# Optimization experiments

Measured on AMD Instinct MI355X. Metric: run time of the kernel, lower is better.

## Reference

```python
import jax, jax.numpy as jnp
import numpy as np

N_NODES = 50000
N_EDGES = 800000
IN_C, HID_C, OUT_C = 256, 256, 128


def gcn_conv(x, W, b, row, col, n_nodes):
    """PyG GCNConv: linear transform, symmetric-normalized aggregation, bias.
    row/col already include self-loops. Messages flow row -> col."""
    h = x @ W  # [N, out]
    deg = jax.ops.segment_sum(jnp.ones_like(col, dtype=h.dtype), col, num_segments=n_nodes)
    d_inv_sqrt = jnp.where(deg > 0, jax.lax.rsqrt(jnp.maximum(deg, 1e-12)), 0.0)
    norm = d_inv_sqrt[row] * d_inv_sqrt[col]  # [E]
    msg = h[row] * norm[:, None]              # gather + scale, [E, out]
    out = jax.ops.segment_sum(msg, col, num_segments=n_nodes)  # scatter-add
    return out + b


def setup_inputs() -> dict:
    key = jax.random.key(0)
    k_x, k_e, k_w1, k_w2 = jax.random.split(key, 4)
    x = jax.random.normal(k_x, (N_NODES, IN_C), dtype=jnp.float32)
    edge_index = jax.random.randint(k_e, (2, N_EDGES), 0, N_NODES, dtype=jnp.int64)
    # Glorot-style init for GCN weights, zeros bias (PyG default)
    s1 = float(np.sqrt(6.0 / (IN_C + HID_C)))
    s2 = float(np.sqrt(6.0 / (HID_C + OUT_C)))
    W1 = jax.random.uniform(k_w1, (IN_C, HID_C), dtype=jnp.float32, minval=-s1, maxval=s1)
    b1 = jnp.zeros((HID_C,), dtype=jnp.float32)
    W2 = jax.random.uniform(k_w2, (HID_C, OUT_C), dtype=jnp.float32, minval=-s2, maxval=s2)
    b2 = jnp.zeros((OUT_C,), dtype=jnp.float32)
    return {"x": x, "edge_index": edge_index, "W1": W1, "b1": b1, "W2": W2, "b2": b2}


def reference(x, edge_index, W1, b1, W2, b2):
    n = x.shape[0]
    # add self-loops (PyG GCNConv default add_self_loops=True)
    loops = jnp.arange(n, dtype=edge_index.dtype)
    row = jnp.concatenate([edge_index[0], loops])
    col = jnp.concatenate([edge_index[1], loops])
    h = gcn_conv(x, W1, b1, row, col, n)
    h = jax.nn.relu(h)  # dropout p=0.0 -> identity
    out = gcn_conv(h, W2, b2, row, col, n)
    return out
```

## Files before the change

### kernel.cpp

```cpp
#include <hip/hip_runtime.h>

#define NN 50000
#define NE 800000
#define IN_C 256
#define HID_C 256
#define OUT_C 128

#define NETP (NE + 8 * NN)
#define NBUCK 196
#define CHUNK 4096
#define NPA 196
#define CAP_B 6400

typedef unsigned short u16;
typedef unsigned int u32;
typedef __attribute__((ext_vector_type(8))) short short8;
typedef __attribute__((ext_vector_type(8))) unsigned short ushort8;
typedef __attribute__((ext_vector_type(4))) float f32x4;
typedef __attribute__((ext_vector_type(2))) float f32x2;
typedef __attribute__((ext_vector_type(4))) unsigned u32x4;

#define CPS ((size_t)(NN + 1) * 32)

__device__ __forceinline__ u16 f2b(float f) {
  unsigned int u = __float_as_uint(f);
  return (u16)((u + 0x7FFFu + ((u >> 16) & 1u)) >> 16);
}
__device__ __forceinline__ float b2f(u16 s) {
  return __uint_as_float(((unsigned int)s) << 16);
}


__global__ __launch_bounds__(256) void convw_zero(const float* __restrict__ W1,
                                                  const float* __restrict__ W2,
                                                  u16* __restrict__ W1t,
                                                  u16* __restrict__ W2t,
                                                  int* __restrict__ cnt,
                                                  u16* __restrict__ Hb,
                                                  int nzb) {
  int b = blockIdx.x;
  if (b < 256) {
    int id = b * 256 + threadIdx.x;
    if (id < 256 * 256) {
      int n = id >> 8, k = id & 255;
      W1t[id] = f2b(W1[k * 256 + n]);
    }
    if (id < 128 * 256) {
      int n = id >> 8, k = id & 255;
      W2t[id] = f2b(W2[k * 128 + n]);
    }
  } else if (b < 256 + nzb) {
    int i = (b - 256) * 256 + threadIdx.x;
    if (i < NN) cnt[i] = 1;
  } else {
    int t = threadIdx.x;
    Hb[(size_t)(t >> 5) * CPS + (size_t)NN * 32 + (t & 31)] = 0;
  }
}


__global__ __launch_bounds__(256) void hist_kernel(const int* __restrict__ col,
                                                   int* __restrict__ cnt, int E) {
  int e = blockIdx.x * blockDim.x + threadIdx.x;
  if (e < E) atomicAdd(&cnt[col[e]], 1);
}

__global__ __launch_bounds__(256) void scan1_kernel(const int* __restrict__ cnt,
                                                    int* __restrict__ bsum, int n) {
  __shared__ int ws[4];
  int i = blockIdx.x * 256 + threadIdx.x;
  int lane = threadIdx.x & 63, wid = threadIdx.x >> 6;
  int v = (i < n) ? ((cnt[i] + 7) & ~7) : 0;
#pragma unroll
  for (int off = 32; off > 0; off >>= 1) v += __shfl_down(v, off, 64);
  if (lane == 0) ws[wid] = v;
  __syncthreads();
  if (threadIdx.x == 0) bsum[blockIdx.x] = ws[0] + ws[1] + ws[2] + ws[3];
}

__global__ __launch_bounds__(256) void scan2_kernel(const int* __restrict__ bsum,
                                                    int* __restrict__ boff,
                                                    int* __restrict__ row_off,
                                                    int nb, int n) {
  __shared__ int wsum[4], wpre[5];
  int lane = threadIdx.x & 63, wid = threadIdx.x >> 6;
  int v = (threadIdx.x < nb) ? bsum[threadIdx.x] : 0;
  int s = v;
#pragma unroll
  for (int off = 1; off < 64; off <<= 1) {
    int t = __shfl_up(s, off, 64);
    if (lane >= off) s += t;
  }
  if (lane == 63) wsum[wid] = s;
  __syncthreads();
  if (threadIdx.x == 0) {
    int acc = 0;
#pragma unroll
    for (int w = 0; w < 4; ++w) { wpre[w] = acc; acc += wsum[w]; }
    wpre[4] = acc;
  }
  __syncthreads();
  if (threadIdx.x < nb) boff[threadIdx.x] = wpre[wid] + (s - v);
  if (threadIdx.x == 0) row_off[n] = wpre[4];
}

__global__ __launch_bounds__(256) void scan3_kernel(const int* __restrict__ cnt,
                                                    const int* __restrict__ boff,
                                                    int* __restrict__ row_off,
                                                    int* __restrict__ bcur,
                                                    float* __restrict__ dinv, int n) {
  __shared__ int wsum[4], wpre[4];
  int i = blockIdx.x * 256 + threadIdx.x;
  int lane = threadIdx.x & 63, wid = threadIdx.x >> 6;
  int vr = (i < n) ? cnt[i] : 0;
  int v = (vr + 7) & ~7;
  int s = v;
#pragma unroll
  for (int off = 1; off < 64; off <<= 1) {
    int t = __shfl_up(s, off, 64);
    if (lane >= off) s += t;
  }
  if (lane == 63) wsum[wid] = s;
  __syncthreads();
  if (threadIdx.x == 0) {
    int acc = 0;
#pragma unroll
    for (int w = 0; w < 4; ++w) { wpre[w] = acc; acc += wsum[w]; }
  }
  __syncthreads();
  if (i < n) {
    int off = boff[blockIdx.x] + wpre[wid] + (s - v);
    row_off[i] = off;
    if ((i & 255) == 0) bcur[i >> 8] = off;
    dinv[i] = rsqrtf((float)vr);
  }
}


template <bool A_IS_F32, bool PLANAR_C>
__device__ __forceinline__ void gemm_body(const void* __restrict__ Ap,
                                          const u16* __restrict__ Bt,
                                          const float* __restrict__ dscale,
                                          u16* __restrict__ C, int M, int N,
                                          int bx, int by,
                                          u16 (&Asl)[2][5120], u16 (&Bsl)[2][5120]) {
  const int tid = threadIdx.x;
  const int row0 = by * 128;
  const int col0 = bx * 128;

  f32x4 acc[4][4] = {};

  const int seg = tid & 7;
  const int rb = tid >> 3;
  const int wave = tid >> 6, lane = tid & 63;
  const int wm = wave >> 1, wn = wave & 1;
  const int qr = lane & 15, quad = lane >> 4;

  float4 aF[4];
  ushort4 aU[4];
  ushort4 bR[4];

  auto load_tiles = [&](int k0) {
    if constexpr (A_IS_F32) {
      const float* A = (const float*)Ap;
#pragma unroll
      for (int i = 0; i < 4; ++i) {
        int gr = row0 + rb + i * 32;
        aF[i] = (gr < M) ? *(const float4*)&A[(size_t)gr * 256 + k0 + seg * 4]
                         : make_float4(0.f, 0.f, 0.f, 0.f);
      }
    } else {
      const u16* A = (const u16*)Ap;
#pragma unroll
      for (int i = 0; i < 4; ++i) {
        int gr = row0 + rb + i * 32;
        aU[i] = (gr < M) ? *(const ushort4*)&A[(size_t)gr * 256 + k0 + seg * 4]
                         : make_ushort4(0, 0, 0, 0);
      }
    }
#pragma unroll
    for (int i = 0; i < 4; ++i) {
      int n = rb + i * 32;
      bR[i] = *(const ushort4*)&Bt[(size_t)(col0 + n) * 256 + k0 + seg * 4];
    }
  };

  auto write_lds = [&](int buf) {
#pragma unroll
    for (int i = 0; i < 4; ++i) {
      int r = rb + i * 32;
      ushort4 u;
      if constexpr (A_IS_F32) {
        u.x = f2b(aF[i].x); u.y = f2b(aF[i].y);
        u.z = f2b(aF[i].z); u.w = f2b(aF[i].w);
      } else {
        u = aU[i];
      }
      *(ushort4*)&Asl[buf][r * 40 + seg * 4] = u;
      *(ushort4*)&Bsl[buf][r * 40 + seg * 4] = bR[i];
    }
  };

  load_tiles(0);
  write_lds(0);
  __syncthreads();

#pragma unroll
  for (int it = 0; it < 8; ++it) {
    const int cur = it & 1;
    if (it < 7) load_tiles((it + 1) * 32);

    short8 afr[4], bfr[4];
#pragma unroll
    for (int mt = 0; mt < 4; ++mt)
      afr[mt] = *(const short8*)&Asl[cur][(wm * 64 + mt * 16 + qr) * 40 + quad * 8];
#pragma unroll
    for (int nt = 0; nt < 4; ++nt)
      bfr[nt] = *(const short8*)&Bsl[cur][(wn * 64 + nt * 16 + qr) * 40 + quad * 8];
#pragma unroll
    for (int mt = 0; mt < 4; ++mt)
#pragma unroll
      for (int nt = 0; nt < 4; ++nt)
        acc[mt][nt] = __builtin_amdgcn_mfma_f32_16x16x32_bf16(afr[mt], bfr[nt], acc[mt][nt], 0, 0, 0);

    if (it < 7) {
      write_lds(1 - cur);
      __syncthreads();
    }
  }

#pragma unroll
  for (int mt = 0; mt < 4; ++mt) {
#pragma unroll
    for (int i = 0; i < 4; ++i) {
      int gr = row0 + wm * 64 + mt * 16 + quad * 4 + i;
      if (gr < M) {
        float sc = dscale[gr];
#pragma unroll
        for (int nt = 0; nt < 4; ++nt) {
          int gc = col0 + wn * 64 + nt * 16 + qr;
          u16 val = f2b(acc[mt][nt][i] * sc);
          if constexpr (PLANAR_C)
            C[(size_t)(gc >> 5) * CPS + (size_t)gr * 32 + (gc & 31)] = val;
          else
            C[(size_t)gr * N + gc] = val;
        }
      }
    }
  }
}

template <bool A_IS_F32, bool PLANAR_C>
__global__ __launch_bounds__(256) void gemm_mfma(const void* __restrict__ Ap,
                                                 const u16* __restrict__ Bt,
                                                 const float* __restrict__ dscale,
                                                 u16* __restrict__ C, int M, int N,
                                                 u16* __restrict__ zrow) {
  if (zrow != nullptr && blockIdx.x == 0 && blockIdx.y == 0 && threadIdx.x < 128) {
    int t = threadIdx.x;
    zrow[(size_t)(t >> 5) * CPS + (size_t)NN * 32 + (t & 31)] = 0;
  }
  __shared__ u16 Asl[2][5120];
  __shared__ u16 Bsl[2][5120];
  gemm_body<A_IS_F32, PLANAR_C>(Ap, Bt, dscale, C, M, N, blockIdx.x, blockIdx.y, Asl, Bsl);
}

__global__ __launch_bounds__(256) void gemm1_scatter(const float* __restrict__ x,
                                                     const u16* __restrict__ W1t,
                                                     const float* __restrict__ dinv,
                                                     u16* __restrict__ Hb, int M, int N,
                                                     int ngb,
                                                     const int* __restrict__ row,
                                                     const int* __restrict__ col,
                                                     int* __restrict__ bcur,
                                                     uint2* __restrict__ stage, int E) {
  __shared__ u16 ABsl[4][5120];
  int b = blockIdx.x;
  if (b < ngb) {
    gemm_body<true, true>(x, W1t, dinv, Hb, M, N, b & 1, b >> 1,
                          *reinterpret_cast<u16(*)[2][5120]>(&ABsl[0]),
                          *reinterpret_cast<u16(*)[2][5120]>(&ABsl[2]));
  } else {
    uint2* pairs = (uint2*)ABsl;
    int* hcnt = (int*)((char*)ABsl + 32768);
    int* hscan = hcnt + 256;
    int* hbase = hscan + 256;
    int* lcur = hbase + 256;

    const int tid = threadIdx.x;
    const int blk = b - ngb;
    const int e0 = blk * CHUNK;

    hcnt[tid] = 0;
    __syncthreads();

    int ecol[16], erow[16];
#pragma unroll
    for (int j = 0; j < 16; ++j) {
      int e = e0 + j * 256 + tid;
      if (e < E) {
        ecol[j] = col[e];
        erow[j] = row[e];
        atomicAdd(&hcnt[ecol[j] >> 8], 1);
      } else {
        ecol[j] = -1;
      }
    }
    __syncthreads();

    hscan[tid] = hcnt[tid];
    __syncthreads();
#pragma unroll
    for (int off = 1; off < 256; off <<= 1) {
      int t = (tid >= off) ? hscan[tid - off] : 0;
      __syncthreads();
      hscan[tid] += t;
      __syncthreads();
    }

    lcur[tid] = 0;
    if (hcnt[tid] > 0) hbase[tid] = atomicAdd(&bcur[tid], hcnt[tid]);
    __syncthreads();

#pragma unroll
    for (int j = 0; j < 16; ++j) {
      if (ecol[j] >= 0) {
        int bk = ecol[j] >> 8;
        int p = atomicAdd(&lcur[bk], 1);
        pairs[(hscan[bk] - hcnt[bk]) + p] = make_uint2((unsigned)erow[j], (unsigned)ecol[j]);
      }
    }
    __syncthreads();

    int mtot = hscan[255];
    for (int s = tid; s < mtot; s += 256) {
      uint2 pr = pairs[s];
      int bk = (int)(pr.y >> 8);
      stage[hbase[bk] + (s - (hscan[bk] - hcnt[bk]))] = pr;
    }
  }
}

__global__ __launch_bounds__(256) void csr_sort(const uint2* __restrict__ stage,
                                                const int* __restrict__ row_off,
                                                const int* __restrict__ bcur,
                                                u16* __restrict__ csrp) {
  __shared__ int cur[256];
  __shared__ u16 outb[CAP_B];
  const int b = blockIdx.x;
  const int base_node = b << 8;
  const int nnodes = min(256, NN - base_node);
  const int tid = threadIdx.x;
  const int bstart = row_off[base_node];
  const int bend = row_off[min(base_node + 256, NN)];
  const int m = bend - bstart;
  const int mm = min(m, CAP_B);
  for (int i = tid; i < mm; i += 256) outb[i] = (u16)NN;
  for (int i = CAP_B + tid; i < m; i += 256) csrp[bstart + i] = (u16)NN;
  __syncthreads();
  if (tid < nnodes) {
    int c0 = row_off[base_node + tid] - bstart;
    outb[c0] = (u16)(base_node + tid);
    cur[tid] = c0 + 1;
  }
  __syncthreads();
  const int mreal = bcur[b] - bstart - 0;
  for (int i = tid; i < mreal; i += 256) {
    uint2 pr = stage[bstart + i];
    int cl = ((int)pr.y - base_node) & 255;
    int p = atomicAdd(&cur[cl], 1);
    if (p < CAP_B) outb[p] = (u16)pr.x;
    else if (bstart + p < NETP) csrp[bstart + p] = (u16)pr.x;
  }
  __syncthreads();
  for (int i = tid; i < mm; i += 256) csrp[bstart + i] = outb[i];
}

template <int NPL, int OUTC, bool RELU_BF16>
__global__ __launch_bounds__(256) void agg_gather(const u16* __restrict__ h,
                                                  const int* __restrict__ row_off,
                                                  const u16* __restrict__ csrp,
                                                  const float* __restrict__ dinv,
                                                  const float* __restrict__ bias,
                                                  void* __restrict__ outp) {
  const int slice = blockIdx.x % NPL;
  const int wave = threadIdx.x >> 6;
  const int lane = threadIdx.x & 63;
  const int nd = lane >> 4;
  const int wg = (lane >> 2) & 3;
  const int c = lane & 3;
  const int v = (blockIdx.x / NPL) * 16 + wave * 4 + nd;
  if (v >= NN) return;
  const u16* hpl = h + (size_t)slice * CPS;
  const int beg = row_off[v], end = row_off[v + 1];
  const int nw = (end - beg) >> 3;
  const int coff = c * 8;

  f32x2 a0 = {}, a1 = {}, a2 = {}, a3 = {};
  for (int w = wg; w < nw; w += 4) {
    ushort8 cw = *(const ushort8*)&csrp[beg + w * 8];
    u32x4 g0 = *(const u32x4*)&hpl[(size_t)cw[0] * 32 + coff];
    u32x4 g1 = *(const u32x4*)&hpl[(size_t)cw[1] * 32 + coff];
    u32x4 g2 = *(const u32x4*)&hpl[(size_t)cw[2] * 32 + coff];
    u32x4 g3 = *(const u32x4*)&hpl[(size_t)cw[3] * 32 + coff];
    u32x4 g4 = *(const u32x4*)&hpl[(size_t)cw[4] * 32 + coff];
    u32x4 g5 = *(const u32x4*)&hpl[(size_t)cw[5] * 32 + coff];
    u32x4 g6 = *(const u32x4*)&hpl[(size_t)cw[6] * 32 + coff];
    u32x4 g7 = *(const u32x4*)&hpl[(size_t)cw[7] * 32 + coff];
#pragma unroll
    for (int q = 0; q < 4; ++q) {
      f32x2 t;
      f32x2 acc = {};
      t[0] = __uint_as_float(g0[q] << 16); t[1] = __uint_as_float(g0[q] & 0xffff0000u); acc += t;
      t[0] = __uint_as_float(g1[q] << 16); t[1] = __uint_as_float(g1[q] & 0xffff0000u); acc += t;
      t[0] = __uint_as_float(g2[q] << 16); t[1] = __uint_as_float(g2[q] & 0xffff0000u); acc += t;
      t[0] = __uint_as_float(g3[q] << 16); t[1] = __uint_as_float(g3[q] & 0xffff0000u); acc += t;
      t[0] = __uint_as_float(g4[q] << 16); t[1] = __uint_as_float(g4[q] & 0xffff0000u); acc += t;
      t[0] = __uint_as_float(g5[q] << 16); t[1] = __uint_as_float(g5[q] & 0xffff0000u); acc += t;
      t[0] = __uint_as_float(g6[q] << 16); t[1] = __uint_as_float(g6[q] & 0xffff0000u); acc += t;
      t[0] = __uint_as_float(g7[q] << 16); t[1] = __uint_as_float(g7[q] & 0xffff0000u); acc += t;
      if (q == 0) a0 += acc;
      else if (q == 1) a1 += acc;
      else if (q == 2) a2 += acc;
      else a3 += acc;
    }
  }
  float aa[8] = {a0[0], a0[1], a1[0], a1[1], a2[0], a2[1], a3[0], a3[1]};
#pragma unroll
  for (int i = 0; i < 8; ++i) {
    aa[i] += __shfl_xor(aa[i], 4, 64);
    aa[i] += __shfl_xor(aa[i], 8, 64);
  }
  if (wg == 0) {
    const int cg = slice * 32 + coff;
    float dv = dinv[v];
    float4 bv0 = *(const float4*)&bias[cg];
    float4 bv1 = *(const float4*)&bias[cg + 4];
    float bb[8] = {bv0.x, bv0.y, bv0.z, bv0.w, bv1.x, bv1.y, bv1.z, bv1.w};
    if constexpr (RELU_BF16) {
      u16* o = (u16*)outp;
      ushort8 ov;
#pragma unroll
      for (int i = 0; i < 8; ++i) ov[i] = (short)f2b(fmaxf(aa[i] * dv + bb[i], 0.f));
      *(ushort8*)&o[(size_t)v * OUTC + cg] = ov;
    } else {
      float* o = (float*)outp;
      float ov[8];
#pragma unroll
      for (int i = 0; i < 8; ++i) ov[i] = aa[i] * dv + bb[i];
      *(float4*)&o[(size_t)v * OUTC + cg] = make_float4(ov[0], ov[1], ov[2], ov[3]);
      *(float4*)&o[(size_t)v * OUTC + cg + 4] = make_float4(ov[4], ov[5], ov[6], ov[7]);
    }
  }
}


extern "C" void kernel_launch(void* const* d_in, const int* in_sizes, int n_in,
                              void* d_out, int out_size, void* d_ws, size_t ws_size,
                              hipStream_t stream) {
  const float* x = (const float*)d_in[0];
  const int* ei = (const int*)d_in[1];
  const float* W1 = (const float*)d_in[2];
  const float* b1 = (const float*)d_in[3];
  const float* W2 = (const float*)d_in[4];
  const float* b2 = (const float*)d_in[5];
  float* out = (float*)d_out;

  const int* row = ei;
  const int* col = ei + NE;

  const int NB = (NN + 255) / 256;

  u16* Hb = (u16*)d_ws;
  u16* H2b = Hb + (size_t)(NN + 1) * 256;
  u16* H3b = H2b + (size_t)NN * 256;
  u16* W1t = H3b + (size_t)(NN + 1) * 128;
  u16* W2t = W1t + 256 * 256;
  int* cnt = (int*)(W2t + 128 * 256);
  int* row_off = cnt + NN;
  int* bcur = row_off + NN + 4;
  float* dinv = (float*)(bcur + 256);
  int* bsum = (int*)(dinv + NN);
  int* boff = bsum + 200;
  u16* csrp = (u16*)(boff + 200);
  uint2* stage = (uint2*)H3b;

  convw_zero<<<256 + NB + 1, 256, 0, stream>>>(W1, W2, W1t, W2t, cnt, Hb, NB);
  hist_kernel<<<(NE + 255) / 256, 256, 0, stream>>>(col, cnt, NE);
  scan1_kernel<<<NB, 256, 0, stream>>>(cnt, bsum, NN);
  scan2_kernel<<<1, 256, 0, stream>>>(bsum, boff, row_off, NB, NN);
  scan3_kernel<<<NB, 256, 0, stream>>>(cnt, boff, row_off, bcur, dinv, NN);

  {
    const int ngb = (HID_C / 128) * ((NN + 127) / 128);
    gemm1_scatter<<<ngb + NPA, 256, 0, stream>>>(x, W1t, dinv, Hb, NN, HID_C, ngb,
                                                 row, col, bcur, stage, NE);
  }
  csr_sort<<<NBUCK, 256, 0, stream>>>(stage, row_off, bcur, csrp);

  const int NGB = (NN + 15) / 16;
  agg_gather<8, 256, true><<<NGB * 8, 256, 0, stream>>>(
      Hb, row_off, csrp, dinv, b1, H2b);

  {
    dim3 grid(OUT_C / 128, (NN + 127) / 128);
    gemm_mfma<false, true><<<grid, 256, 0, stream>>>(H2b, W2t, dinv, H3b, NN, OUT_C, H3b);
  }

  agg_gather<4, 128, false><<<NGB * 4, 256, 0, stream>>>(
      H3b, row_off, csrp, dinv, b2, out);
}
```

Before: 265.9 us.

## Precompute per-chunk bucket offsets to make edge staging deterministic

Adds a pre-pass that histograms each edge chunk into destination buckets and a per-bucket scan that gives every chunk a fixed write offset. The scatter phase then reads its base from this table instead of claiming space with global atomics. Staged edges land in chunk order, which may give csr_sort a more regular input. The cost is two extra kernel launches and one more full read of the column indices.

```diff
diff --git a/kernel.cpp b/kernel.cpp
--- a/kernel.cpp
+++ b/kernel.cpp
@@ -65,6 +65,51 @@
   if (e < E) atomicAdd(&cnt[col[e]], 1);
 }
 
+__global__ __launch_bounds__(256) void passA_hist(const int* __restrict__ col,
+                                                  int* __restrict__ cntmat, int E) {
+  __shared__ int hcnt[256];
+  const int blk = blockIdx.x;
+  const int tid = threadIdx.x;
+  hcnt[tid] = 0;
+  __syncthreads();
+  const int e0 = blk * CHUNK;
+#pragma unroll
+  for (int j = 0; j < 16; ++j) {
+    int e = e0 + j * 256 + tid;
+    if (e < E) atomicAdd(&hcnt[col[e] >> 8], 1);
+  }
+  __syncthreads();
+  cntmat[tid * 256 + blk] = hcnt[tid];
+}
+
+__global__ __launch_bounds__(256) void passA_scan(const int* __restrict__ cntmat,
+                                                  const int* __restrict__ row_off,
+                                                  int* __restrict__ gbase,
+                                                  int* __restrict__ btot) {
+  __shared__ int wsum[4], wpre[4];
+  const int b = blockIdx.x;
+  const int tid = threadIdx.x;
+  int lane = tid & 63, wid = tid >> 6;
+  int v = (tid < NPA) ? cntmat[b * 256 + tid] : 0;
+  int s = v;
+#pragma unroll
+  for (int off = 1; off < 64; off <<= 1) {
+    int t = __shfl_up(s, off, 64);
+    if (lane >= off) s += t;
+  }
+  if (lane == 63) wsum[wid] = s;
+  __syncthreads();
+  if (tid == 0) {
+    int acc = 0;
+#pragma unroll
+    for (int w = 0; w < 4; ++w) { wpre[w] = acc; acc += wsum[w]; }
+  }
+  __syncthreads();
+  int bstart = row_off[b << 8];
+  gbase[b * 256 + tid] = bstart + wpre[wid] + (s - v);
+  if (tid == 255) btot[b] = wpre[3] + s;
+}
+
 __global__ __launch_bounds__(256) void scan1_kernel(const int* __restrict__ cnt,
                                                     int* __restrict__ bsum, int n) {
   __shared__ int ws[4];
@@ -107,7 +152,6 @@
 __global__ __launch_bounds__(256) void scan3_kernel(const int* __restrict__ cnt,
                                                     const int* __restrict__ boff,
                                                     int* __restrict__ row_off,
-                                                    int* __restrict__ bcur,
                                                     float* __restrict__ dinv, int n) {
   __shared__ int wsum[4], wpre[4];
   int i = blockIdx.x * 256 + threadIdx.x;
@@ -131,7 +175,6 @@
   if (i < n) {
     int off = boff[blockIdx.x] + wpre[wid] + (s - v);
     row_off[i] = off;
-    if ((i & 255) == 0) bcur[i >> 8] = off;
     dinv[i] = rsqrtf((float)vr);
   }
 }
@@ -272,7 +315,7 @@
                                                      int ngb,
                                                      const int* __restrict__ row,
                                                      const int* __restrict__ col,
-                                                     int* __restrict__ bcur,
+                                                     const int* __restrict__ gbase,
                                                      uint2* __restrict__ stage, int E) {
   __shared__ u16 ABsl[4][5120];
   int b = blockIdx.x;
@@ -319,7 +362,7 @@
     }
 
     lcur[tid] = 0;
-    if (hcnt[tid] > 0) hbase[tid] = atomicAdd(&bcur[tid], hcnt[tid]);
+    hbase[tid] = gbase[tid * 256 + blk];
     __syncthreads();
 
 #pragma unroll
@@ -343,7 +386,7 @@
 
 __global__ __launch_bounds__(256) void csr_sort(const uint2* __restrict__ stage,
                                                 const int* __restrict__ row_off,
-                                                const int* __restrict__ bcur,
+                                                const int* __restrict__ btot,
                                                 u16* __restrict__ csrp) {
   __shared__ int cur[256];
   __shared__ u16 outb[CAP_B];
@@ -364,7 +407,7 @@
     cur[tid] = c0 + 1;
   }
   __syncthreads();
-  const int mreal = bcur[b] - bstart - 0;
+  const int mreal = btot[b];
   for (int i = tid; i < mreal; i += 256) {
     uint2 pr = stage[bstart + i];
     int cl = ((int)pr.y - base_node) & 255;
@@ -478,25 +521,29 @@
   u16* W2t = W1t + 256 * 256;
   int* cnt = (int*)(W2t + 128 * 256);
   int* row_off = cnt + NN;
-  int* bcur = row_off + NN + 4;
-  float* dinv = (float*)(bcur + 256);
+  float* dinv = (float*)(row_off + NN + 4);
   int* bsum = (int*)(dinv + NN);
   int* boff = bsum + 200;
-  u16* csrp = (u16*)(boff + 200);
+  int* cntmat = boff + 200;
+  int* gbase = cntmat + 256 * 256;
+  int* btot = gbase + 256 * 256;
+  u16* csrp = (u16*)(btot + 256);
   uint2* stage = (uint2*)H3b;
 
   convw_zero<<<256 + NB + 1, 256, 0, stream>>>(W1, W2, W1t, W2t, cnt, Hb, NB);
+  passA_hist<<<NPA, 256, 0, stream>>>(col, cntmat, NE);
   hist_kernel<<<(NE + 255) / 256, 256, 0, stream>>>(col, cnt, NE);
   scan1_kernel<<<NB, 256, 0, stream>>>(cnt, bsum, NN);
   scan2_kernel<<<1, 256, 0, stream>>>(bsum, boff, row_off, NB, NN);
-  scan3_kernel<<<NB, 256, 0, stream>>>(cnt, boff, row_off, bcur, dinv, NN);
+  scan3_kernel<<<NB, 256, 0, stream>>>(cnt, boff, row_off, dinv, NN);
+  passA_scan<<<NBUCK, 256, 0, stream>>>(cntmat, row_off, gbase, btot);
 
   {
     const int ngb = (HID_C / 128) * ((NN + 127) / 128);
     gemm1_scatter<<<ngb + NPA, 256, 0, stream>>>(x, W1t, dinv, Hb, NN, HID_C, ngb,
-                                                 row, col, bcur, stage, NE);
-  }
-  csr_sort<<<NBUCK, 256, 0, stream>>>(stage, row_off, bcur, csrp);
+                                                 row, col, gbase, stage, NE);
+  }
+  csr_sort<<<NBUCK, 256, 0, stream>>>(stage, row_off, btot, csrp);
 
   const int NGB = (NN + 15) / 16;
   agg_gather<8, 256, true><<<NGB * 8, 256, 0, stream>>>(
```

Measured after the change: 274.1 us. +3.1%, slower.
